# Kernel tuning notes

Measured on AMD Instinct MI355X. Metric: run time of the kernel, lower is better.

Reference implementation:

```python
import jax, jax.numpy as jnp
import numpy as np

N_NODES = 100000
N_EDGES = 800000
IN_DIM = 128
HID_DIM = 128
OUT_DIM = 128


def setup_inputs() -> dict:
    key = jax.random.key(0)
    ks = jax.random.split(key, 10)
    feat1 = jax.random.normal(ks[0], (N_NODES, IN_DIM), dtype=jnp.float32)
    feat2 = jax.random.normal(ks[1], (N_NODES, IN_DIM), dtype=jnp.float32)
    # GraphConv weights (Glorot-ish scale) and biases
    W1 = jax.random.normal(ks[2], (IN_DIM, HID_DIM), dtype=jnp.float32) * (1.0 / np.sqrt(IN_DIM))
    b1 = jnp.zeros((HID_DIM,), dtype=jnp.float32)
    W2 = jax.random.normal(ks[3], (HID_DIM, OUT_DIM), dtype=jnp.float32) * (1.0 / np.sqrt(HID_DIM))
    b2 = jnp.zeros((OUT_DIM,), dtype=jnp.float32)
    src1 = jax.random.randint(ks[4], (N_EDGES,), 0, N_NODES, dtype=jnp.int32)
    dst1 = jax.random.randint(ks[5], (N_EDGES,), 0, N_NODES, dtype=jnp.int32)
    src2 = jax.random.randint(ks[6], (N_EDGES,), 0, N_NODES, dtype=jnp.int32)
    dst2 = jax.random.randint(ks[7], (N_EDGES,), 0, N_NODES, dtype=jnp.int32)
    return {"feat1": feat1, "feat2": feat2, "W1": W1, "b1": b1, "W2": W2, "b2": b2,
            "src1": src1, "dst1": dst1, "src2": src2, "dst2": dst2}


def _graph_conv(x, src, dst, W, b, n_nodes):
    # DGL GraphConv, norm='both': h = D_in^{-1/2} A D_out^{-1/2} x W + b
    ones = jnp.ones(src.shape, dtype=x.dtype)
    deg_out = jax.ops.segment_sum(ones, src, num_segments=n_nodes)
    deg_in = jax.ops.segment_sum(ones, dst, num_segments=n_nodes)
    x = x * (jnp.maximum(deg_out, 1.0) ** -0.5)[:, None]
    x = x @ W                                 # apply linear before aggregation (equivalent math)
    agg = jax.ops.segment_sum(x[src], dst, num_segments=n_nodes)  # SpMM: gather + scatter-add
    return agg * (jnp.maximum(deg_in, 1.0) ** -0.5)[:, None] + b


def _encode(x, src, dst, Ws, bs, n_nodes):
    for i in range(len(Ws) - 1):
        x = jax.nn.relu(_graph_conv(x, src, dst, Ws[i], bs[i], n_nodes))
    return _graph_conv(x, src, dst, Ws[-1], bs[-1], n_nodes)


def reference(feat1, feat2, W1, b1, W2, b2, src1, dst1, src2, dst2):
    n = feat1.shape[0]
    Ws, bs = [W1, W2], [b1, b2]
    h1 = _encode(feat1, src1, dst1, Ws, bs, n)
    h2 = _encode(feat2, src2, dst2, Ws, bs, n)
    # per-feature z-score; torch std(0) is unbiased (ddof=1)
    z1 = (h1 - h1.mean(0)) / h1.std(0, ddof=1)
    z2 = (h2 - h2.mean(0)) / h2.std(0, ddof=1)
    return (z1, z2)
```

## Files before the change

### kernel.cpp

```cpp
#include <hip/hip_runtime.h>
#include <cstdint>
#include <cstddef>


#define SCAN_CHUNK 1024
#define NSLICES 64
#define HWORDS 25000

typedef __attribute__((ext_vector_type(8))) short bf16x8;
typedef __attribute__((ext_vector_type(4))) float f32x4;

__device__ __forceinline__ unsigned short f2bf(float f) {
    unsigned int u = __float_as_uint(f);
    unsigned int r = (u + 0x7FFFu + ((u >> 16) & 1u)) >> 16;
    return (unsigned short)r;
}
__device__ __forceinline__ float bflo(unsigned int u) { return __uint_as_float(u << 16); }
__device__ __forceinline__ float bfhi(unsigned int u) { return __uint_as_float(u & 0xffff0000u); }

__global__ __launch_bounds__(1024) void hist_kernel(
    const int* __restrict__ src1, const int* __restrict__ dst1,
    const int* __restrict__ src2, const int* __restrict__ dst2,
    unsigned int* __restrict__ part, int E)
{
    __shared__ unsigned int h[HWORDS];
    const int bid = blockIdx.x;
    const int a = bid / NSLICES, s = bid % NSLICES;
    const int* idx = a == 0 ? src1 : a == 1 ? dst1 : a == 2 ? src2 : dst2;

    for (int i = threadIdx.x; i < HWORDS; i += 1024) h[i] = 0u;
    __syncthreads();

    const int lo = (int)((long long)s * E / NSLICES);
    const int hi = (int)((long long)(s + 1) * E / NSLICES);
    for (int i = lo + threadIdx.x; i < hi; i += 1024) {
        unsigned int v = (unsigned int)idx[i];
        atomicAdd(&h[v >> 2], 1u << ((v & 3u) << 3));
    }
    __syncthreads();

    unsigned int* out = part + (size_t)bid * HWORDS;
    for (int i = threadIdx.x; i < HWORDS; i += 1024) out[i] = h[i];
}

__global__ __launch_bounds__(256) void hist_reduce(
    const unsigned int* __restrict__ part, int* __restrict__ deg, int M)
{
    int i = blockIdx.x * blockDim.x + threadIdx.x;
    if (i >= 4 * HWORDS) return;
    int a = i / HWORDS, w = i % HWORDS;
    const unsigned int* p = part + (size_t)a * NSLICES * HWORDS + w;
    unsigned int accA = 0u, accB = 0u;
#pragma unroll
    for (int s = 0; s < NSLICES; ++s) {
        unsigned int v = p[(size_t)s * HWORDS];
        accA += v & 0x00FF00FFu;
        accB += (v >> 8) & 0x00FF00FFu;
    }
    int4 r = make_int4((int)(accA & 0xFFFFu), (int)(accB & 0xFFFFu),
                       (int)(accA >> 16),     (int)(accB >> 16));
    *(int4*)(deg + (size_t)a * M + 4 * w) = r;
}

__global__ void scan_block_sums(const int* __restrict__ deg, int* __restrict__ partials, int M)
{
    __shared__ int sd[256];
    int base = blockIdx.x * SCAN_CHUNK + threadIdx.x * 4;
    int s = 0;
#pragma unroll
    for (int j = 0; j < 4; ++j) { int i = base + j; if (i < M) s += deg[i]; }
    sd[threadIdx.x] = s;
    __syncthreads();
    for (int off = 128; off > 0; off >>= 1) {
        if (threadIdx.x < off) sd[threadIdx.x] += sd[threadIdx.x + off];
        __syncthreads();
    }
    if (threadIdx.x == 0) partials[blockIdx.x] = sd[0];
}

__global__ void scan_partials(const int* __restrict__ partials, int* __restrict__ blockoff, int P)
{
    __shared__ int sd[256];
    int v = threadIdx.x < P ? partials[threadIdx.x] : 0;
    sd[threadIdx.x] = v;
    __syncthreads();
    for (int off = 1; off < 256; off <<= 1) {
        int t = threadIdx.x >= off ? sd[threadIdx.x - off] : 0;
        __syncthreads();
        sd[threadIdx.x] += t;
        __syncthreads();
    }
    if (threadIdx.x < P) blockoff[threadIdx.x] = sd[threadIdx.x] - v;
}

__global__ void scan_write(const int* __restrict__ deg, const int* __restrict__ blockoff,
                           int* __restrict__ rowptr, int* __restrict__ cursor, int M)
{
    __shared__ int sd[256];
    int base = blockIdx.x * SCAN_CHUNK + threadIdx.x * 4;
    int d0 = 0, d1 = 0, d2 = 0, d3 = 0;
    if (base + 0 < M) d0 = deg[base + 0];
    if (base + 1 < M) d1 = deg[base + 1];
    if (base + 2 < M) d2 = deg[base + 2];
    if (base + 3 < M) d3 = deg[base + 3];
    int tot = d0 + d1 + d2 + d3;
    sd[threadIdx.x] = tot;
    __syncthreads();
    for (int off = 1; off < 256; off <<= 1) {
        int t = threadIdx.x >= off ? sd[threadIdx.x - off] : 0;
        __syncthreads();
        sd[threadIdx.x] += t;
        __syncthreads();
    }
    int texcl = sd[threadIdx.x] - tot + blockoff[blockIdx.x];
    int p0 = texcl + d0, p1 = p0 + d1, p2 = p1 + d2, p3 = p2 + d3;
    if (base + 0 < M) { rowptr[base + 1] = p0; cursor[base + 0] = texcl; }
    if (base + 1 < M) { rowptr[base + 2] = p1; cursor[base + 1] = p0; }
    if (base + 2 < M) { rowptr[base + 3] = p2; cursor[base + 2] = p1; }
    if (base + 3 < M) { rowptr[base + 4] = p3; cursor[base + 3] = p2; }
    if (blockIdx.x == 0 && threadIdx.x == 0) rowptr[0] = 0;
}

__global__ void csr_fill(const int* __restrict__ src, const int* __restrict__ dst,
                         int* __restrict__ cursor, int* __restrict__ colidx, int E)
{
    int e = blockIdx.x * blockDim.x + threadIdx.x;
    if (e >= E) return;
    int pos = atomicAdd(&cursor[dst[e]], 1);
    colidx[pos] = src[e];
}

__global__ void wswz_kernel(const float* __restrict__ W, unsigned short* __restrict__ Wz)
{
    int i = blockIdx.x * 256 + threadIdx.x;
    int j = i & 7, l = (i >> 3) & 63, s = (i >> 9) & 3, t = i >> 11;
    int k = s * 32 + ((l >> 4) * 8) + j;
    int n = t * 16 + (l & 15);
    Wz[i] = f2bf(W[k * 128 + n]);
}

__global__ __launch_bounds__(256) void mfma_gemm(
    const float* __restrict__ X, const unsigned short* __restrict__ Wz,
    const int* __restrict__ deg_out, unsigned short* __restrict__ Yh, int M)
{
    __shared__ __align__(16) unsigned short Abf[64 * 136];
    const int tid  = threadIdx.x;
    const int row0 = blockIdx.x * 64;

#pragma unroll
    for (int i = 0; i < 8; ++i) {
        int idx = tid + i * 256;
        int r = idx >> 5, c4 = idx & 31;
        int gr = row0 + r;
        float4 v = make_float4(0.f, 0.f, 0.f, 0.f);
        if (gr < M) {
            v = ((const float4*)X)[(size_t)gr * 32 + c4];
            float so = rsqrtf(fmaxf((float)deg_out[gr], 1.f));
            v.x *= so; v.y *= so; v.z *= so; v.w *= so;
        }
        unsigned int lo = (unsigned int)f2bf(v.x) | ((unsigned int)f2bf(v.y) << 16);
        unsigned int hi = (unsigned int)f2bf(v.z) | ((unsigned int)f2bf(v.w) << 16);
        *(uint2*)(Abf + r * 136 + c4 * 4) = make_uint2(lo, hi);
    }
    __syncthreads();

    const int w = tid >> 6, lane = tid & 63;
    const int m = lane & 15, quad = lane >> 4;

    bf16x8 a[4];
#pragma unroll
    for (int s = 0; s < 4; ++s)
        a[s] = *(const bf16x8*)(Abf + (w * 16 + m) * 136 + s * 32 + quad * 8);

#pragma unroll
    for (int t = 0; t < 8; ++t) {
        f32x4 acc = {0.f, 0.f, 0.f, 0.f};
#pragma unroll
        for (int s = 0; s < 4; ++s) {
            bf16x8 b = *(const bf16x8*)(Wz + (((t * 4 + s) * 64 + lane) << 3));
            acc = __builtin_amdgcn_mfma_f32_16x16x32_bf16(a[s], b, acc, 0, 0, 0);
        }
        int gr  = row0 + w * 16 + quad * 4;
        int col = t * 16 + m;
#pragma unroll
        for (int r = 0; r < 4; ++r) {
            if (gr + r < M) Yh[(size_t)(gr + r) * 128 + col] = f2bf(acc[r]);
        }
    }
}

#define G16_ACC(v)                                                              \
    a0 += bflo(v.x); a1 += bfhi(v.x); a2 += bflo(v.y); a3 += bfhi(v.y);         \
    a4 += bflo(v.z); a5 += bfhi(v.z); a6 += bflo(v.w); a7 += bfhi(v.w);

#define GATHER_ROW16                                                            \
    {                                                                           \
        for (; e + 8 <= end; e += 8) {                                          \
            int c0 = colidx[e+0], c1 = colidx[e+1], c2 = colidx[e+2], c3 = colidx[e+3]; \
            int c4_ = colidx[e+4], c5 = colidx[e+5], c6 = colidx[e+6], c7 = colidx[e+7]; \
            uint4 v0 = Yv[(size_t)c0 * 16 + lane16];                            \
            uint4 v1 = Yv[(size_t)c1 * 16 + lane16];                            \
            uint4 v2 = Yv[(size_t)c2 * 16 + lane16];                            \
            uint4 v3 = Yv[(size_t)c3 * 16 + lane16];                            \
            uint4 v4 = Yv[(size_t)c4_ * 16 + lane16];                           \
            uint4 v5 = Yv[(size_t)c5 * 16 + lane16];                            \
            uint4 v6 = Yv[(size_t)c6 * 16 + lane16];                            \
            uint4 v7 = Yv[(size_t)c7 * 16 + lane16];                            \
            G16_ACC(v0) G16_ACC(v1) G16_ACC(v2) G16_ACC(v3)                     \
            G16_ACC(v4) G16_ACC(v5) G16_ACC(v6) G16_ACC(v7)                     \
        }                                                                       \
        if (e + 4 <= end) {                                                     \
            int c0 = colidx[e+0], c1 = colidx[e+1], c2 = colidx[e+2], c3 = colidx[e+3]; \
            uint4 v0 = Yv[(size_t)c0 * 16 + lane16];                            \
            uint4 v1 = Yv[(size_t)c1 * 16 + lane16];                            \
            uint4 v2 = Yv[(size_t)c2 * 16 + lane16];                            \
            uint4 v3 = Yv[(size_t)c3 * 16 + lane16];                            \
            G16_ACC(v0) G16_ACC(v1) G16_ACC(v2) G16_ACC(v3)                     \
            e += 4;                                                             \
        }                                                                       \
        for (; e < end; ++e) {                                                  \
            int c = colidx[e];                                                  \
            uint4 v = Yv[(size_t)c * 16 + lane16];                              \
            G16_ACC(v)                                                          \
        }                                                                       \
    }

__global__ __launch_bounds__(256) void spmm_gemm(
    const uint4* __restrict__ Yv, const int* __restrict__ rowptr,
    const int* __restrict__ colidx, const unsigned short* __restrict__ Wz,
    const int* __restrict__ deg_out, const int* __restrict__ deg_in,
    const float* __restrict__ bias, unsigned short* __restrict__ Yh2, int M)
{
    __shared__ __align__(16) unsigned short Abf[64 * 136];
    const int tid  = threadIdx.x;
    const int row0 = blockIdx.x * 64;
    const int lane16 = tid & 15;
    const int ng = tid >> 4;
    const float4 bv0 = ((const float4*)bias)[lane16 * 2];
    const float4 bv1 = ((const float4*)bias)[lane16 * 2 + 1];

#pragma unroll 1
    for (int p = 0; p < 4; ++p) {
        const int r = p * 16 + ng;
        const int node = row0 + r;
        float a0=0.f,a1=0.f,a2=0.f,a3=0.f,a4=0.f,a5=0.f,a6=0.f,a7=0.f;
        if (node < M) {
            int e = rowptr[node], end = rowptr[node + 1];
            GATHER_ROW16
            float si = rsqrtf(fmaxf((float)deg_in[node], 1.f));
            float so = rsqrtf(fmaxf((float)deg_out[node], 1.f));
            a0 = fmaxf(a0 * si + bv0.x, 0.f) * so;
            a1 = fmaxf(a1 * si + bv0.y, 0.f) * so;
            a2 = fmaxf(a2 * si + bv0.z, 0.f) * so;
            a3 = fmaxf(a3 * si + bv0.w, 0.f) * so;
            a4 = fmaxf(a4 * si + bv1.x, 0.f) * so;
            a5 = fmaxf(a5 * si + bv1.y, 0.f) * so;
            a6 = fmaxf(a6 * si + bv1.z, 0.f) * so;
            a7 = fmaxf(a7 * si + bv1.w, 0.f) * so;
        }
        uint4 wv;
        wv.x = (unsigned int)f2bf(a0) | ((unsigned int)f2bf(a1) << 16);
        wv.y = (unsigned int)f2bf(a2) | ((unsigned int)f2bf(a3) << 16);
        wv.z = (unsigned int)f2bf(a4) | ((unsigned int)f2bf(a5) << 16);
        wv.w = (unsigned int)f2bf(a6) | ((unsigned int)f2bf(a7) << 16);
        *(uint4*)(Abf + r * 136 + lane16 * 8) = wv;
    }
    __syncthreads();

    const int w = tid >> 6, lane = tid & 63;
    const int m = lane & 15, quad = lane >> 4;

    bf16x8 a[4];
#pragma unroll
    for (int s = 0; s < 4; ++s)
        a[s] = *(const bf16x8*)(Abf + (w * 16 + m) * 136 + s * 32 + quad * 8);

#pragma unroll
    for (int t = 0; t < 8; ++t) {
        f32x4 acc = {0.f, 0.f, 0.f, 0.f};
#pragma unroll
        for (int s = 0; s < 4; ++s) {
            bf16x8 b = *(const bf16x8*)(Wz + (((t * 4 + s) * 64 + lane) << 3));
            acc = __builtin_amdgcn_mfma_f32_16x16x32_bf16(a[s], b, acc, 0, 0, 0);
        }
        int gr  = row0 + w * 16 + quad * 4;
        int col = t * 16 + m;
#pragma unroll
        for (int r = 0; r < 4; ++r) {
            if (gr + r < M) Yh2[(size_t)(gr + r) * 128 + col] = f2bf(acc[r]);
        }
    }
}

__global__ __launch_bounds__(256) void spmm_stats(
    const uint4* __restrict__ Yv, const int* __restrict__ rowptr,
    const int* __restrict__ colidx, const int* __restrict__ deg_in,
    const float* __restrict__ bias, float* __restrict__ Z,
    double* __restrict__ gsum, double* __restrict__ gsumsq, int M)
{
    __shared__ float lsum[16][128], lsq[16][128];
    const int tid  = threadIdx.x;
    const int row0 = blockIdx.x * 64;
    const int lane16 = tid & 15;
    const int ng = tid >> 4;
    const float4 bv0 = ((const float4*)bias)[lane16 * 2];
    const float4 bv1 = ((const float4*)bias)[lane16 * 2 + 1];

    float s0=0.f,s1=0.f,s2=0.f,s3=0.f,s4=0.f,s5=0.f,s6=0.f,s7=0.f;
    float q0=0.f,q1=0.f,q2=0.f,q3=0.f,q4=0.f,q5=0.f,q6=0.f,q7=0.f;

#pragma unroll 1
    for (int p = 0; p < 4; ++p) {
        const int node = row0 + p * 16 + ng;
        if (node >= M) continue;
        float a0=0.f,a1=0.f,a2=0.f,a3=0.f,a4=0.f,a5=0.f,a6=0.f,a7=0.f;
        int e = rowptr[node], end = rowptr[node + 1];
        GATHER_ROW16
        float si = rsqrtf(fmaxf((float)deg_in[node], 1.f));
        float h0 = a0 * si + bv0.x, h1 = a1 * si + bv0.y;
        float h2 = a2 * si + bv0.z, h3 = a3 * si + bv0.w;
        float h4 = a4 * si + bv1.x, h5 = a5 * si + bv1.y;
        float h6 = a6 * si + bv1.z, h7 = a7 * si + bv1.w;
        ((float4*)Z)[(size_t)node * 32 + lane16 * 2]     = make_float4(h0, h1, h2, h3);
        ((float4*)Z)[(size_t)node * 32 + lane16 * 2 + 1] = make_float4(h4, h5, h6, h7);
        s0 += h0; s1 += h1; s2 += h2; s3 += h3;
        s4 += h4; s5 += h5; s6 += h6; s7 += h7;
        q0 += h0*h0; q1 += h1*h1; q2 += h2*h2; q3 += h3*h3;
        q4 += h4*h4; q5 += h5*h5; q6 += h6*h6; q7 += h7*h7;
    }

    const int cb = lane16 * 8;
    lsum[ng][cb+0]=s0; lsum[ng][cb+1]=s1; lsum[ng][cb+2]=s2; lsum[ng][cb+3]=s3;
    lsum[ng][cb+4]=s4; lsum[ng][cb+5]=s5; lsum[ng][cb+6]=s6; lsum[ng][cb+7]=s7;
    lsq[ng][cb+0]=q0; lsq[ng][cb+1]=q1; lsq[ng][cb+2]=q2; lsq[ng][cb+3]=q3;
    lsq[ng][cb+4]=q4; lsq[ng][cb+5]=q5; lsq[ng][cb+6]=q6; lsq[ng][cb+7]=q7;
    __syncthreads();

    if (tid < 128) {
        float s = 0.f;
#pragma unroll
        for (int g = 0; g < 16; ++g) s += lsum[g][tid];
        atomicAdd(&gsum[tid], (double)s);
    } else {
        int c = tid - 128;
        float q = 0.f;
#pragma unroll
        for (int g = 0; g < 16; ++g) q += lsq[g][c];
        atomicAdd(&gsumsq[c], (double)q);
    }
}

__global__ void meanstd_kernel(const double* __restrict__ gsum,
                               const double* __restrict__ gsumsq, int M,
                               float* __restrict__ mean, float* __restrict__ istd)
{
    int c = threadIdx.x;
    double mu  = gsum[c] / (double)M;
    double var = (gsumsq[c] - gsum[c] * mu) / (double)(M - 1);
    mean[c] = (float)mu;
    istd[c] = (float)(1.0 / sqrt(var));
}

__global__ __launch_bounds__(256) void normalize_kernel(
    float* __restrict__ Z, const float* __restrict__ mean,
    const float* __restrict__ istd, int n4)
{
    int i = blockIdx.x * blockDim.x + threadIdx.x;
    if (i >= n4) return;
    float4 v = ((float4*)Z)[i];
    int c4 = (i & 31) << 2;
    v.x = (v.x - mean[c4 + 0]) * istd[c4 + 0];
    v.y = (v.y - mean[c4 + 1]) * istd[c4 + 1];
    v.z = (v.z - mean[c4 + 2]) * istd[c4 + 2];
    v.w = (v.w - mean[c4 + 3]) * istd[c4 + 3];
    ((float4*)Z)[i] = v;
}

extern "C" void kernel_launch(void* const* d_in, const int* in_sizes, int n_in,
                              void* d_out, int out_size, void* d_ws, size_t ws_size,
                              hipStream_t stream)
{
    const float* feat1 = (const float*)d_in[0];
    const float* feat2 = (const float*)d_in[1];
    const float* W1    = (const float*)d_in[2];
    const float* b1    = (const float*)d_in[3];
    const float* W2    = (const float*)d_in[4];
    const float* b2    = (const float*)d_in[5];
    const int*   src1  = (const int*)d_in[6];
    const int*   dst1  = (const int*)d_in[7];
    const int*   src2  = (const int*)d_in[8];
    const int*   dst2  = (const int*)d_in[9];
    float* out = (float*)d_out;

    const int M = in_sizes[0] / 128;
    const int E = in_sizes[6];

    double* gsum = (double*)d_ws;
    double* gsq  = gsum + 128;
    float* scratch = (float*)(gsq + 128);
    unsigned short* Yh = (unsigned short*)(scratch + (size_t)M * 128);
    unsigned short* Wz = Yh + (size_t)M * 128;
    float*  mean = (float*)(Wz + 32768);
    float*  istd = mean + 128;
    int*    deg  = (int*)(istd + 128);
    int*  rowptr = deg + (size_t)4 * M;
    int*  cursor = rowptr + (M + 1);
    int*  colidx = cursor + M;
    int* spart   = colidx + E;
    int* blockoff = spart + 256;

    int* do1 = deg;
    int* di1 = deg + M;
    int* do2 = deg + 2 * M;
    int* di2 = deg + 3 * M;
    unsigned short* Wz1 = Wz;
    unsigned short* Wz2 = Wz + 16384;

    unsigned int* hpart = (unsigned int*)scratch;
    unsigned short* Yh2 = (unsigned short*)(scratch + (size_t)M * 64);

    const int BLK = 256;
    const int gemm_blocks = (M + 63) / 64;
    const int P = (M + SCAN_CHUNK - 1) / SCAN_CHUNK;
    const int hist_blocks = 4 * NSLICES;
    const int hr_total = 4 * HWORDS;

    hist_kernel<<<hist_blocks, 1024, 0, stream>>>(src1, dst1, src2, dst2, hpart, E);
    hist_reduce<<<(hr_total + BLK - 1) / BLK, BLK, 0, stream>>>(hpart, deg, M);
    wswz_kernel<<<64, BLK, 0, stream>>>(W1, Wz1);
    wswz_kernel<<<64, BLK, 0, stream>>>(W2, Wz2);

    for (int g = 0; g < 2; ++g) {
        const float* feat = g == 0 ? feat1 : feat2;
        const int* src = g == 0 ? src1 : src2;
        const int* dst = g == 0 ? dst1 : dst2;
        const int* dgo = g == 0 ? do1 : do2;
        const int* dgi = g == 0 ? di1 : di2;
        float* Zg = out + (size_t)g * M * 128;

        scan_block_sums<<<P, BLK, 0, stream>>>(dgi, spart, M);
        scan_partials<<<1, BLK, 0, stream>>>(spart, blockoff, P);
        scan_write<<<P, BLK, 0, stream>>>(dgi, blockoff, rowptr, cursor, M);
        csr_fill<<<(E + BLK - 1) / BLK, BLK, 0, stream>>>(src, dst, cursor, colidx, E);

        mfma_gemm<<<gemm_blocks, BLK, 0, stream>>>(feat, Wz1, dgo, Yh, M);

        spmm_gemm<<<gemm_blocks, BLK, 0, stream>>>(
            (const uint4*)Yh, rowptr, colidx, Wz2, dgo, dgi, b1, Yh2, M);

        hipMemsetAsync(gsum, 0, 2 * 128 * sizeof(double), stream);
        spmm_stats<<<gemm_blocks, BLK, 0, stream>>>(
            (const uint4*)Yh2, rowptr, colidx, dgi, b2, Zg, gsum, gsq, M);

        meanstd_kernel<<<1, 128, 0, stream>>>(gsum, gsq, M, mean, istd);
        normalize_kernel<<<(M * 32 + BLK - 1) / BLK, BLK, 0, stream>>>(Zg, mean, istd, M * 32);
    }
}
```

Before: 614.4 us.

## Batch both graph pipelines into shared launches via a second grid dimension

Every stage (scan, CSR fill, GEMM, SpMM+GEMM, SpMM+stats, normalize) now handles both graphs in one launch, using blockIdx.y to pick per-graph pointers. The two weight swizzles are also merged into one kernel. The workspace is re-laid out with separate per-graph CSR and intermediate buffers, and falls back to the old one-graph-at-a-time loop when the workspace is too small. The aim is to halve launch count and serialization gaps, and to fill the GPU better in the small scan and stat kernels, at the cost of more workspace memory and a larger combined cache footprint.

```diff
diff --git a/kernel.cpp b/kernel.cpp
--- a/kernel.cpp
+++ b/kernel.cpp
@@ -62,26 +62,32 @@
     *(int4*)(deg + (size_t)a * M + 4 * w) = r;
 }
 
-__global__ void scan_block_sums(const int* __restrict__ deg, int* __restrict__ partials, int M)
+__global__ void scan_block_sums(const int* __restrict__ deg, int* __restrict__ partials,
+                                int M, int goff)
 {
     __shared__ int sd[256];
+    const int g = blockIdx.y + goff;
+    const int* d = deg + (size_t)(2 * g + 1) * M;
     int base = blockIdx.x * SCAN_CHUNK + threadIdx.x * 4;
     int s = 0;
 #pragma unroll
-    for (int j = 0; j < 4; ++j) { int i = base + j; if (i < M) s += deg[i]; }
+    for (int j = 0; j < 4; ++j) { int i = base + j; if (i < M) s += d[i]; }
     sd[threadIdx.x] = s;
     __syncthreads();
     for (int off = 128; off > 0; off >>= 1) {
         if (threadIdx.x < off) sd[threadIdx.x] += sd[threadIdx.x + off];
         __syncthreads();
     }
-    if (threadIdx.x == 0) partials[blockIdx.x] = sd[0];
-}
-
-__global__ void scan_partials(const int* __restrict__ partials, int* __restrict__ blockoff, int P)
+    if (threadIdx.x == 0) partials[g * 256 + blockIdx.x] = sd[0];
+}
+
+__global__ void scan_partials(const int* __restrict__ partials, int* __restrict__ blockoff,
+                              int P, int goff)
 {
     __shared__ int sd[256];
-    int v = threadIdx.x < P ? partials[threadIdx.x] : 0;
+    const int g = blockIdx.y + goff;
+    const int* pp = partials + g * 256;
+    int v = threadIdx.x < P ? pp[threadIdx.x] : 0;
     sd[threadIdx.x] = v;
     __syncthreads();
     for (int off = 1; off < 256; off <<= 1) {
@@ -90,19 +96,23 @@
         sd[threadIdx.x] += t;
         __syncthreads();
     }
-    if (threadIdx.x < P) blockoff[threadIdx.x] = sd[threadIdx.x] - v;
+    if (threadIdx.x < P) blockoff[g * 256 + threadIdx.x] = sd[threadIdx.x] - v;
 }
 
 __global__ void scan_write(const int* __restrict__ deg, const int* __restrict__ blockoff,
-                           int* __restrict__ rowptr, int* __restrict__ cursor, int M)
+                           int* rp0, int* rp1, int* cu0, int* cu1, int M, int goff)
 {
     __shared__ int sd[256];
+    const int g = blockIdx.y + goff;
+    const int* d = deg + (size_t)(2 * g + 1) * M;
+    int* rowptr = g ? rp1 : rp0;
+    int* cursor = g ? cu1 : cu0;
     int base = blockIdx.x * SCAN_CHUNK + threadIdx.x * 4;
     int d0 = 0, d1 = 0, d2 = 0, d3 = 0;
-    if (base + 0 < M) d0 = deg[base + 0];
-    if (base + 1 < M) d1 = deg[base + 1];
-    if (base + 2 < M) d2 = deg[base + 2];
-    if (base + 3 < M) d3 = deg[base + 3];
+    if (base + 0 < M) d0 = d[base + 0];
+    if (base + 1 < M) d1 = d[base + 1];
+    if (base + 2 < M) d2 = d[base + 2];
+    if (base + 3 < M) d3 = d[base + 3];
     int tot = d0 + d1 + d2 + d3;
     sd[threadIdx.x] = tot;
     __syncthreads();
@@ -112,7 +122,7 @@
         sd[threadIdx.x] += t;
         __syncthreads();
     }
-    int texcl = sd[threadIdx.x] - tot + blockoff[blockIdx.x];
+    int texcl = sd[threadIdx.x] - tot + blockoff[g * 256 + blockIdx.x];
     int p0 = texcl + d0, p1 = p0 + d1, p2 = p1 + d2, p3 = p2 + d3;
     if (base + 0 < M) { rowptr[base + 1] = p0; cursor[base + 0] = texcl; }
     if (base + 1 < M) { rowptr[base + 2] = p1; cursor[base + 1] = p0; }
@@ -121,29 +131,42 @@
     if (blockIdx.x == 0 && threadIdx.x == 0) rowptr[0] = 0;
 }
 
-__global__ void csr_fill(const int* __restrict__ src, const int* __restrict__ dst,
-                         int* __restrict__ cursor, int* __restrict__ colidx, int E)
-{
+__global__ void csr_fill(const int* s0, const int* s1, const int* d0, const int* d1,
+                         int* cu0, int* cu1, int* co0, int* co1, int E, int goff)
+{
+    const int g = blockIdx.y + goff;
+    const int* src = g ? s1 : s0;
+    const int* dst = g ? d1 : d0;
+    int* cursor = g ? cu1 : cu0;
+    int* colidx = g ? co1 : co0;
     int e = blockIdx.x * blockDim.x + threadIdx.x;
     if (e >= E) return;
     int pos = atomicAdd(&cursor[dst[e]], 1);
     colidx[pos] = src[e];
 }
 
-__global__ void wswz_kernel(const float* __restrict__ W, unsigned short* __restrict__ Wz)
+__global__ void wswz_kernel(const float* __restrict__ Wa, const float* __restrict__ Wb,
+                            unsigned short* __restrict__ Wz)
 {
     int i = blockIdx.x * 256 + threadIdx.x;
-    int j = i & 7, l = (i >> 3) & 63, s = (i >> 9) & 3, t = i >> 11;
+    const float* W = (i < 16384) ? Wa : Wb;
+    int ii = i & 16383;
+    int j = ii & 7, l = (ii >> 3) & 63, s = (ii >> 9) & 3, t = ii >> 11;
     int k = s * 32 + ((l >> 4) * 8) + j;
     int n = t * 16 + (l & 15);
     Wz[i] = f2bf(W[k * 128 + n]);
 }
 
 __global__ __launch_bounds__(256) void mfma_gemm(
-    const float* __restrict__ X, const unsigned short* __restrict__ Wz,
-    const int* __restrict__ deg_out, unsigned short* __restrict__ Yh, int M)
+    const float* X0, const float* X1, const unsigned short* __restrict__ Wz,
+    const int* __restrict__ deg, unsigned short* Y0, unsigned short* Y1,
+    int M, int goff)
 {
     __shared__ __align__(16) unsigned short Abf[64 * 136];
+    const int g = blockIdx.y + goff;
+    const float* X = g ? X1 : X0;
+    const int* deg_out = deg + (size_t)2 * g * M;
+    unsigned short* Yh = g ? Y1 : Y0;
     const int tid  = threadIdx.x;
     const int row0 = blockIdx.x * 64;
 
@@ -226,12 +249,20 @@
     }
 
 __global__ __launch_bounds__(256) void spmm_gemm(
-    const uint4* __restrict__ Yv, const int* __restrict__ rowptr,
-    const int* __restrict__ colidx, const unsigned short* __restrict__ Wz,
-    const int* __restrict__ deg_out, const int* __restrict__ deg_in,
-    const float* __restrict__ bias, unsigned short* __restrict__ Yh2, int M)
+    const uint4* Y0, const uint4* Y1, const int* rp0, const int* rp1,
+    const int* ci0, const int* ci1, const unsigned short* __restrict__ Wz,
+    const int* __restrict__ deg, const float* __restrict__ bias,
+    unsigned short* O0, unsigned short* O1, int M, int goff)
 {
     __shared__ __align__(16) unsigned short Abf[64 * 136];
+    const int g = blockIdx.y + goff;
+    const uint4* Yv = g ? Y1 : Y0;
+    const int* rowptr = g ? rp1 : rp0;
+    const int* colidx = g ? ci1 : ci0;
+    const int* deg_out = deg + (size_t)2 * g * M;
+    const int* deg_in  = deg_out + M;
+    unsigned short* Yh2 = g ? O1 : O0;
+
     const int tid  = threadIdx.x;
     const int row0 = blockIdx.x * 64;
     const int lane16 = tid & 15;
@@ -293,12 +324,21 @@
 }
 
 __global__ __launch_bounds__(256) void spmm_stats(
-    const uint4* __restrict__ Yv, const int* __restrict__ rowptr,
-    const int* __restrict__ colidx, const int* __restrict__ deg_in,
+    const uint4* Y0, const uint4* Y1, const int* rp0, const int* rp1,
+    const int* ci0, const int* ci1, const int* __restrict__ deg,
     const float* __restrict__ bias, float* __restrict__ Z,
-    double* __restrict__ gsum, double* __restrict__ gsumsq, int M)
+    double* __restrict__ gsum, double* __restrict__ gsumsq, int M, int goff)
 {
     __shared__ float lsum[16][128], lsq[16][128];
+    const int g = blockIdx.y + goff;
+    const uint4* Yv = g ? Y1 : Y0;
+    const int* rowptr = g ? rp1 : rp0;
+    const int* colidx = g ? ci1 : ci0;
+    const int* deg_in = deg + (size_t)(2 * g + 1) * M;
+    float* Zg = Z + (size_t)g * M * 128;
+    double* gs = gsum + g * 128;
+    double* gq = gsumsq + g * 128;
+
     const int tid  = threadIdx.x;
     const int row0 = blockIdx.x * 64;
     const int lane16 = tid & 15;
@@ -321,8 +361,8 @@
         float h2 = a2 * si + bv0.z, h3 = a3 * si + bv0.w;
         float h4 = a4 * si + bv1.x, h5 = a5 * si + bv1.y;
         float h6 = a6 * si + bv1.z, h7 = a7 * si + bv1.w;
-        ((float4*)Z)[(size_t)node * 32 + lane16 * 2]     = make_float4(h0, h1, h2, h3);
-        ((float4*)Z)[(size_t)node * 32 + lane16 * 2 + 1] = make_float4(h4, h5, h6, h7);
+        ((float4*)Zg)[(size_t)node * 32 + lane16 * 2]     = make_float4(h0, h1, h2, h3);
+        ((float4*)Zg)[(size_t)node * 32 + lane16 * 2 + 1] = make_float4(h4, h5, h6, h7);
         s0 += h0; s1 += h1; s2 += h2; s3 += h3;
         s4 += h4; s5 += h5; s6 += h6; s7 += h7;
         q0 += h0*h0; q1 += h1*h1; q2 += h2*h2; q3 += h3*h3;
@@ -339,14 +379,14 @@
     if (tid < 128) {
         float s = 0.f;
 #pragma unroll
-        for (int g = 0; g < 16; ++g) s += lsum[g][tid];
-        atomicAdd(&gsum[tid], (double)s);
+        for (int g2 = 0; g2 < 16; ++g2) s += lsum[g2][tid];
+        atomicAdd(&gs[tid], (double)s);
     } else {
         int c = tid - 128;
         float q = 0.f;
 #pragma unroll
-        for (int g = 0; g < 16; ++g) q += lsq[g][c];
-        atomicAdd(&gsumsq[c], (double)q);
+        for (int g2 = 0; g2 < 16; ++g2) q += lsq[g2][c];
+        atomicAdd(&gq[c], (double)q);
     }
 }
 
@@ -363,12 +403,13 @@
 
 __global__ __launch_bounds__(256) void normalize_kernel(
     float* __restrict__ Z, const float* __restrict__ mean,
-    const float* __restrict__ istd, int n4)
+    const float* __restrict__ istd, int n4_per_g, int n4tot)
 {
     int i = blockIdx.x * blockDim.x + threadIdx.x;
-    if (i >= n4) return;
+    if (i >= n4tot) return;
+    int gb = (i >= n4_per_g) ? 128 : 0;
     float4 v = ((float4*)Z)[i];
-    int c4 = (i & 31) << 2;
+    int c4 = gb + ((i & 31) << 2);
     v.x = (v.x - mean[c4 + 0]) * istd[c4 + 0];
     v.y = (v.y - mean[c4 + 1]) * istd[c4 + 1];
     v.z = (v.z - mean[c4 + 2]) * istd[c4 + 2];
@@ -395,64 +436,92 @@
     const int M = in_sizes[0] / 128;
     const int E = in_sizes[6];
 
-    double* gsum = (double*)d_ws;
-    double* gsq  = gsum + 128;
-    float* scratch = (float*)(gsq + 128);
-    unsigned short* Yh = (unsigned short*)(scratch + (size_t)M * 128);
-    unsigned short* Wz = Yh + (size_t)M * 128;
-    float*  mean = (float*)(Wz + 32768);
-    float*  istd = mean + 128;
-    int*    deg  = (int*)(istd + 128);
-    int*  rowptr = deg + (size_t)4 * M;
-    int*  cursor = rowptr + (M + 1);
-    int*  colidx = cursor + M;
-    int* spart   = colidx + E;
-    int* blockoff = spart + 256;
-
-    int* do1 = deg;
-    int* di1 = deg + M;
-    int* do2 = deg + 2 * M;
-    int* di2 = deg + 3 * M;
+    char* p0 = (char*)d_ws;
+    char* p = p0;
+    auto alloc = [&](size_t b) -> char* {
+        char* r = p; p += (b + 255) & ~(size_t)255; return r;
+    };
+
+    double* gsum = (double*)alloc(256 * 8);
+    double* gsq  = (double*)alloc(256 * 8);
+    float*  mean = (float*)alloc(256 * 4);
+    float*  istd = (float*)alloc(256 * 4);
+    unsigned short* Wz = (unsigned short*)alloc(32768 * 2);
+    int* deg = (int*)alloc((size_t)4 * M * 4);
+    int* spart = (int*)alloc(512 * 4);
+    int* blockoff = (int*)alloc(512 * 4);
+
+    const size_t bytesRP = (size_t)(M + 1) * 4;
+    const size_t bytesCU = (size_t)M * 4;
+    const size_t bytesCI = (size_t)E * 4;
+    const size_t bytesYh = (size_t)M * 128 * 2;
+    const size_t bytesHP = (size_t)4 * NSLICES * HWORDS * 4;
+
+    size_t fixed = (size_t)(p - p0);
+    size_t need_merged = fixed + 2 * ((bytesRP + 255 & ~(size_t)255) +
+                                      (bytesCU + 255 & ~(size_t)255) +
+                                      (bytesCI + 255 & ~(size_t)255) +
+                                      2 * ((bytesYh + 255 & ~(size_t)255)));
+    const bool merged = ws_size >= need_merged + 4096;
+
+    int *rpA, *rpB, *cuA, *cuB, *ciA, *ciB;
+    unsigned short *YhA0, *YhA1, *YhB0, *YhB1;
+    unsigned int* hpart;
+
+    if (merged) {
+        rpA = (int*)alloc(bytesRP);  rpB = (int*)alloc(bytesRP);
+        cuA = (int*)alloc(bytesCU);  cuB = (int*)alloc(bytesCU);
+        ciA = (int*)alloc(bytesCI);  ciB = (int*)alloc(bytesCI);
+        YhA0 = (unsigned short*)alloc(bytesYh);
+        YhA1 = (unsigned short*)alloc(bytesYh);
+        YhB0 = (unsigned short*)alloc(bytesYh);
+        YhB1 = (unsigned short*)alloc(bytesYh);
+        hpart = (unsigned int*)YhA0;
+    } else {
+        rpA = (int*)alloc(bytesRP);  rpB = rpA;
+        cuA = (int*)alloc(bytesCU);  cuB = cuA;
+        ciA = (int*)alloc(bytesCI);  ciB = ciA;
+        YhA0 = (unsigned short*)alloc(bytesYh);  YhA1 = YhA0;
+        char* scratch = alloc(bytesHP + bytesYh);
+        hpart = (unsigned int*)scratch;
+        YhB0 = (unsigned short*)(scratch + bytesHP); YhB1 = YhB0;
+    }
+
     unsigned short* Wz1 = Wz;
     unsigned short* Wz2 = Wz + 16384;
-
-    unsigned int* hpart = (unsigned int*)scratch;
-    unsigned short* Yh2 = (unsigned short*)(scratch + (size_t)M * 64);
 
     const int BLK = 256;
     const int gemm_blocks = (M + 63) / 64;
     const int P = (M + SCAN_CHUNK - 1) / SCAN_CHUNK;
-    const int hist_blocks = 4 * NSLICES;
-    const int hr_total = 4 * HWORDS;
-
-    hist_kernel<<<hist_blocks, 1024, 0, stream>>>(src1, dst1, src2, dst2, hpart, E);
-    hist_reduce<<<(hr_total + BLK - 1) / BLK, BLK, 0, stream>>>(hpart, deg, M);
-    wswz_kernel<<<64, BLK, 0, stream>>>(W1, Wz1);
-    wswz_kernel<<<64, BLK, 0, stream>>>(W2, Wz2);
-
-    for (int g = 0; g < 2; ++g) {
-        const float* feat = g == 0 ? feat1 : feat2;
-        const int* src = g == 0 ? src1 : src2;
-        const int* dst = g == 0 ? dst1 : dst2;
-        const int* dgo = g == 0 ? do1 : do2;
-        const int* dgi = g == 0 ? di1 : di2;
-        float* Zg = out + (size_t)g * M * 128;
-
-        scan_block_sums<<<P, BLK, 0, stream>>>(dgi, spart, M);
-        scan_partials<<<1, BLK, 0, stream>>>(spart, blockoff, P);
-        scan_write<<<P, BLK, 0, stream>>>(dgi, blockoff, rowptr, cursor, M);
-        csr_fill<<<(E + BLK - 1) / BLK, BLK, 0, stream>>>(src, dst, cursor, colidx, E);
-
-        mfma_gemm<<<gemm_blocks, BLK, 0, stream>>>(feat, Wz1, dgo, Yh, M);
-
-        spmm_gemm<<<gemm_blocks, BLK, 0, stream>>>(
-            (const uint4*)Yh, rowptr, colidx, Wz2, dgo, dgi, b1, Yh2, M);
-
-        hipMemsetAsync(gsum, 0, 2 * 128 * sizeof(double), stream);
-        spmm_stats<<<gemm_blocks, BLK, 0, stream>>>(
-            (const uint4*)Yh2, rowptr, colidx, dgi, b2, Zg, gsum, gsq, M);
-
-        meanstd_kernel<<<1, 128, 0, stream>>>(gsum, gsq, M, mean, istd);
-        normalize_kernel<<<(M * 32 + BLK - 1) / BLK, BLK, 0, stream>>>(Zg, mean, istd, M * 32);
-    }
-}
+    const int NG = merged ? 2 : 1;
+
+    hist_kernel<<<4 * NSLICES, 1024, 0, stream>>>(src1, dst1, src2, dst2, hpart, E);
+    hist_reduce<<<(4 * HWORDS + BLK - 1) / BLK, BLK, 0, stream>>>(hpart, deg, M);
+    wswz_kernel<<<128, BLK, 0, stream>>>(W1, W2, Wz);
+
+    for (int g0 = 0; g0 < 2; g0 += NG) {
+        dim3 gP(P, NG), gE((E + BLK - 1) / BLK, NG), gG(gemm_blocks, NG);
+
+        scan_block_sums<<<gP, BLK, 0, stream>>>(deg, spart, M, g0);
+        scan_partials<<<dim3(1, NG), BLK, 0, stream>>>(spart, blockoff, P, g0);
+        scan_write<<<gP, BLK, 0, stream>>>(deg, blockoff, rpA, rpB, cuA, cuB, M, g0);
+        csr_fill<<<gE, BLK, 0, stream>>>(src1, src2, dst1, dst2, cuA, cuB, ciA, ciB, E, g0);
+
+        mfma_gemm<<<gG, BLK, 0, stream>>>(feat1, feat2, Wz1, deg, YhA0, YhA1, M, g0);
+
+        spmm_gemm<<<gG, BLK, 0, stream>>>(
+            (const uint4*)YhA0, (const uint4*)YhA1, rpA, rpB, ciA, ciB,
+            Wz2, deg, b1, YhB0, YhB1, M, g0);
+
+        hipMemsetAsync(gsum, 0, 2 * 256 * sizeof(double), stream);
+        spmm_stats<<<gG, BLK, 0, stream>>>(
+            (const uint4*)YhB0, (const uint4*)YhB1, rpA, rpB, ciA, ciB,
+            deg, b2, out, gsum, gsq, M, g0);
+
+        meanstd_kernel<<<1, NG * 128, 0, stream>>>(
+            gsum + g0 * 128, gsq + g0 * 128, M, mean + g0 * 128, istd + g0 * 128);
+        int n4g = M * 32, n4tot = NG * n4g;
+        normalize_kernel<<<(n4tot + BLK - 1) / BLK, BLK, 0, stream>>>(
+            out + (size_t)g0 * M * 128, mean + g0 * 128, istd + g0 * 128, n4g, n4tot);
+    }
+}
```

Result: faster. 598.2 us (-2.6%).
